# Kernel tuning notes

Measured on AMD Instinct MI355X. Metric: run time of the kernel, lower is better.

## Reference

```python
import jax, jax.numpy as jnp
import numpy as np

D_MODEL = 1024
NUM_HEADS = 16
HEAD_DIM = D_MODEL // NUM_HEADS


def setup_inputs() -> dict:
    key = jax.random.key(0)
    ks = jax.random.split(key, 9)
    s = 1.0 / np.sqrt(D_MODEL)
    x = jax.random.normal(ks[0], (2, 2048, D_MODEL), dtype=jnp.float32)
    Wq = jax.random.normal(ks[1], (D_MODEL, D_MODEL), dtype=jnp.float32) * s
    bq = jnp.zeros((D_MODEL,), dtype=jnp.float32)
    Wk = jax.random.normal(ks[2], (D_MODEL, D_MODEL), dtype=jnp.float32) * s
    bk = jnp.zeros((D_MODEL,), dtype=jnp.float32)
    Wv = jax.random.normal(ks[3], (D_MODEL, D_MODEL), dtype=jnp.float32) * s
    bv = jnp.zeros((D_MODEL,), dtype=jnp.float32)
    Wo = jax.random.normal(ks[4], (D_MODEL, D_MODEL), dtype=jnp.float32) * s
    bo = jnp.zeros((D_MODEL,), dtype=jnp.float32)
    return {"x": x, "Wq": Wq, "bq": bq, "Wk": Wk, "bk": bk,
            "Wv": Wv, "bv": bv, "Wo": Wo, "bo": bo}


def reference(x, Wq, bq, Wk, bk, Wv, bv, Wo, bo):
    B, S, D = x.shape
    H, Hd = NUM_HEADS, HEAD_DIM
    scale = 1.0 / np.sqrt(Hd)

    def split_heads(t):  # [B,S,D] -> [B,H,S,Hd]
        return t.reshape(B, S, H, Hd).transpose(0, 2, 1, 3)

    q = split_heads(x @ Wq + bq)
    k = split_heads(x @ Wk + bk)
    v = split_heads(x @ Wv + bv)

    scores = jnp.einsum('bhqd,bhkd->bhqk', q, k) * scale
    scores = scores - jnp.max(scores, axis=-1, keepdims=True)
    attn = jax.nn.softmax(scores, axis=-1)
    attended = jnp.einsum('bhqk,bhkd->bhqd', attn, v)
    attended = attended.transpose(0, 2, 1, 3).reshape(B, S, D)
    return attended @ Wo + bo
```

## Files before the change

### kernel.cpp

```cpp
#include <hip/hip_runtime.h>
#include <hip/hip_bf16.h>

typedef __bf16 bf16_t;
typedef __bf16 bf16x8 __attribute__((ext_vector_type(8)));
typedef __bf16 bf16x4 __attribute__((ext_vector_type(4)));
typedef float floatx4 __attribute__((ext_vector_type(4)));
typedef short short4v __attribute__((ext_vector_type(4)));

#define D_MODEL 1024
#define SEQ     2048
#define BATCH   2
#define NHEAD   16
#define HDIM    64
#define MTOT    (BATCH * SEQ)

#define QSCALE  0.18033688011112042f

union PBu { bf16x4 b; short4v s; };

__device__ __forceinline__ void async_copy16(const bf16_t* g, bf16_t* l) {
    __builtin_amdgcn_global_load_lds(
        (const __attribute__((address_space(1))) void*)g,
        (__attribute__((address_space(3))) void*)l, 16, 0, 0);
}

__global__ void prep_kernel(
    const float* __restrict__ x, bf16_t* __restrict__ xb,
    const float* __restrict__ W0, const float* __restrict__ W1,
    const float* __restrict__ W2, const float* __restrict__ W3,
    bf16_t* __restrict__ T0, bf16_t* __restrict__ T1,
    bf16_t* __restrict__ T2, bf16_t* __restrict__ T3)
{
    const int z = blockIdx.z;
    const int tx = threadIdx.x, ty = threadIdx.y;
    if (z == 4) {
        const int lin = (blockIdx.y * 32 + blockIdx.x) * 256 + ty * 32 + tx;
        const int base = lin * 16;
#pragma unroll
        for (int c = 0; c < 4; ++c) {
            const float4 v = *(const float4*)(x + base + c * 4);
            bf16x4 o = { (bf16_t)v.x, (bf16_t)v.y, (bf16_t)v.z, (bf16_t)v.w };
            *(bf16x4*)(xb + base + c * 4) = o;
        }
        return;
    }
    __shared__ float tile[32][33];
    const float* W = (z == 0) ? W0 : (z == 1) ? W1 : (z == 2) ? W2 : W3;
    bf16_t*     Wt = (z == 0) ? T0 : (z == 1) ? T1 : (z == 2) ? T2 : T3;
    const int k0 = blockIdx.y * 32, n0 = blockIdx.x * 32;
#pragma unroll
    for (int j = 0; j < 32; j += 8)
        tile[ty + j][tx] = W[(size_t)(k0 + ty + j) * D_MODEL + n0 + tx];
    __syncthreads();
#pragma unroll
    for (int j = 0; j < 32; j += 8)
        Wt[(size_t)(n0 + ty + j) * D_MODEL + k0 + tx] = (bf16_t)tile[tx][ty + j];
}

__device__ __forceinline__ void gemm_mainloop(
    const bf16_t* __restrict__ A, const bf16_t* __restrict__ Bt,
    int m0, int n0, bf16_t* As, bf16_t* Bs, floatx4 acc[4][4])
{
    const int tid  = threadIdx.x;
    const int lane = tid & 63;
    const int wid  = tid >> 6;
    const int quad = lane >> 4;
    const int col  = lane & 15;
    const int wm   = (wid >> 1) * 64;
    const int wn   = (wid & 1) * 64;
    const int srow = tid >> 3;
    const int scc  = ((tid & 7) ^ (srow & 7)) * 8;
    const int xorc = col & 7;

    const bf16_t* Ag = A  + (size_t)(m0 + srow) * D_MODEL + scc;
    const bf16_t* Bg = Bt + (size_t)(n0 + srow) * D_MODEL + scc;
    bf16_t* Al = As + tid * 8;
    bf16_t* Bl = Bs + tid * 8;

    for (int kb = 0; kb < D_MODEL; kb += 64) {
#pragma unroll
        for (int p = 0; p < 4; ++p) {
            async_copy16(Ag + kb + p * (32 * D_MODEL), Al + p * 2048);
            async_copy16(Bg + kb + p * (32 * D_MODEL), Bl + p * 2048);
        }
        __syncthreads();
#pragma unroll
        for (int kh = 0; kh < 2; ++kh) {
            bf16x8 af[4], bfr[4];
#pragma unroll
            for (int i = 0; i < 4; ++i)
                af[i] = *(const bf16x8*)(As + (wm + i * 16 + col) * 64 + (((kh * 4 + quad) ^ xorc) * 8));
#pragma unroll
            for (int j = 0; j < 4; ++j)
                bfr[j] = *(const bf16x8*)(Bs + (wn + j * 16 + col) * 64 + (((kh * 4 + quad) ^ xorc) * 8));
#pragma unroll
            for (int i = 0; i < 4; ++i)
#pragma unroll
                for (int j = 0; j < 4; ++j)
                    acc[i][j] = __builtin_amdgcn_mfma_f32_16x16x32_bf16(af[i], bfr[j], acc[i][j], 0, 0, 0);
        }
        __syncthreads();
    }
}

__global__ __launch_bounds__(256, 3) void gemm_qkv(
    const bf16_t* __restrict__ xb,
    const bf16_t* __restrict__ Wtq, const bf16_t* __restrict__ Wtk, const bf16_t* __restrict__ Wtv,
    const float* __restrict__ bq, const float* __restrict__ bk, const float* __restrict__ bv,
    bf16_t* __restrict__ Q, bf16_t* __restrict__ Kh, bf16_t* __restrict__ Vt)
{
    __shared__ bf16_t As[128 * 64];
    __shared__ bf16_t Bs[128 * 64];
    const int z = blockIdx.z;
    const bf16_t* Bt   = (z == 0) ? Wtq : (z == 1) ? Wtk : Wtv;
    const float*  bias = (z == 0) ? bq  : (z == 1) ? bk  : bv;
    bf16_t*       O    = (z == 0) ? Q   : (z == 1) ? Kh  : Vt;
    const float   qs   = (z == 0) ? QSCALE : 1.0f;
    const int m0 = blockIdx.y * 128;
    const int n0 = blockIdx.x * 128;

    floatx4 acc[4][4];
#pragma unroll
    for (int i = 0; i < 4; ++i)
#pragma unroll
        for (int j = 0; j < 4; ++j)
            acc[i][j] = (floatx4){0.f, 0.f, 0.f, 0.f};

    gemm_mainloop(xb, Bt, m0, n0, As, Bs, acc);

    const int tid  = threadIdx.x;
    const int lane = tid & 63;
    const int wid  = tid >> 6;
    const int quad = lane >> 4;
    const int col  = lane & 15;
    const int wm   = (wid >> 1) * 64;
    const int wn   = (wid & 1) * 64;

    if (z == 2) {
#pragma unroll
        for (int i = 0; i < 4; ++i) {
#pragma unroll
            for (int j = 0; j < 4; ++j) {
                const int n = n0 + wn + j * 16 + col;
                const float bb = bias[n];
                const int mb = m0 + wm + i * 16 + quad * 4;
                const size_t bhb = (size_t)((mb >> 11) * NHEAD + (n >> 6)) * (SEQ * HDIM);
                bf16x4 pk = { (bf16_t)(acc[i][j][0] + bb), (bf16_t)(acc[i][j][1] + bb),
                              (bf16_t)(acc[i][j][2] + bb), (bf16_t)(acc[i][j][3] + bb) };
                *(bf16x4*)(O + bhb + (size_t)(n & 63) * SEQ + (mb & 2047)) = pk;
            }
        }
    } else {
#pragma unroll
        for (int i = 0; i < 4; ++i) {
#pragma unroll
            for (int j = 0; j < 4; ++j) {
                const int n = n0 + wn + j * 16 + col;
                const float bb = bias[n];
#pragma unroll
                for (int r = 0; r < 4; ++r) {
                    const int m = m0 + wm + i * 16 + quad * 4 + r;
                    const float v = (acc[i][j][r] + bb) * qs;
                    const size_t bhb = (size_t)((m >> 11) * NHEAD + (n >> 6)) * (SEQ * HDIM);
                    O[bhb + (size_t)(m & 2047) * HDIM + (n & 63)] = (bf16_t)v;
                }
            }
        }
    }
}

__global__ __launch_bounds__(256, 4) void attn_kernel(
    const bf16_t* __restrict__ Q, const bf16_t* __restrict__ K,
    const bf16_t* __restrict__ Vt, bf16_t* __restrict__ A2)
{
    __shared__ bf16_t Ks[2][64 * 64];
    __shared__ bf16_t Vs[2][64 * 64];

    const int tid  = threadIdx.x;
    const int lane = tid & 63;
    const int wid  = tid >> 6;
    const int quad = lane >> 4;
    const int col  = lane & 15;
    const int xorc = col & 7;

    const int blk = blockIdx.x;
    const int idx = blk >> 3;
    const int bh  = (blk & 7) * 4 + (idx >> 5);
    const int q0  = (idx & 31) * 64;
    const int b   = bh >> 4, h = bh & 15;

    const bf16_t* Qb = Q  + (size_t)bh * (SEQ * HDIM);
    const bf16_t* Kb = K  + (size_t)bh * (SEQ * HDIM);
    const bf16_t* Vb = Vt + (size_t)bh * (SEQ * HDIM);

    const int qrow = q0 + wid * 16 + col;
    bf16x8 qf0 = *(const bf16x8*)(Qb + (size_t)qrow * HDIM + quad * 8);
    bf16x8 qf1 = *(const bf16x8*)(Qb + (size_t)qrow * HDIM + 32 + quad * 8);

    floatx4 o_acc[4];
    float lsum = 0.f;
#pragma unroll
    for (int dt = 0; dt < 4; ++dt)
        o_acc[dt] = (floatx4){0.f, 0.f, 0.f, 0.f};

    const int srow = tid >> 3;
    const int scc  = ((tid & 7) ^ (srow & 7)) * 8;
    const bf16_t* Kg = Kb + (size_t)srow * HDIM + scc;
    const bf16_t* Vg = Vb + (size_t)srow * SEQ + scc;

    async_copy16(Kg, &Ks[0][tid * 8]);
    async_copy16(Kg + (size_t)32 * HDIM, &Ks[0][2048 + tid * 8]);
    async_copy16(Vg, &Vs[0][tid * 8]);
    async_copy16(Vg + (size_t)32 * SEQ, &Vs[0][2048 + tid * 8]);
    __syncthreads();

    for (int it = 0; it < 32; ++it) {
        const int cur = it & 1, nxt = cur ^ 1;
        if (it + 1 < 32) {
            const int ko = (it + 1) * 64;
            async_copy16(Kg + (size_t)ko * HDIM, &Ks[nxt][tid * 8]);
            async_copy16(Kg + (size_t)(ko + 32) * HDIM, &Ks[nxt][2048 + tid * 8]);
            async_copy16(Vg + ko, &Vs[nxt][tid * 8]);
            async_copy16(Vg + (size_t)32 * SEQ + ko, &Vs[nxt][2048 + tid * 8]);
        }
        const bf16_t* Kc = Ks[cur];
        const bf16_t* Vc = Vs[cur];

        bf16x8 kf[4][2];
#pragma unroll
        for (int t = 0; t < 4; ++t) {
            kf[t][0] = *(const bf16x8*)(Kc + (t * 16 + col) * 64 + ((quad ^ xorc) * 8));
            kf[t][1] = *(const bf16x8*)(Kc + (t * 16 + col) * 64 + (((4 + quad) ^ xorc) * 8));
        }
        short4v vfr[4][4];
#pragma unroll
        for (int dt = 0; dt < 4; ++dt)
#pragma unroll
            for (int t = 0; t < 4; ++t) {
                const int sch = t * 2 + (quad >> 1);
                vfr[dt][t] = *(const short4v*)(Vc + (dt * 16 + col) * 64 + ((sch ^ xorc) * 8) + (quad & 1) * 4);
            }

        floatx4 s_acc[4];
        short4v pb[4];
#pragma unroll
        for (int t = 0; t < 4; ++t) {
            s_acc[t] = (floatx4){0.f, 0.f, 0.f, 0.f};
            s_acc[t] = __builtin_amdgcn_mfma_f32_16x16x32_bf16(kf[t][0], qf0, s_acc[t], 0, 0, 0);
            s_acc[t] = __builtin_amdgcn_mfma_f32_16x16x32_bf16(kf[t][1], qf1, s_acc[t], 0, 0, 0);
        }
#pragma unroll
        for (int t = 0; t < 4; ++t) {
            const float p0 = __builtin_amdgcn_exp2f(s_acc[t][0]);
            const float p1 = __builtin_amdgcn_exp2f(s_acc[t][1]);
            const float p2 = __builtin_amdgcn_exp2f(s_acc[t][2]);
            const float p3 = __builtin_amdgcn_exp2f(s_acc[t][3]);
            lsum += (p0 + p1) + (p2 + p3);
            PBu u;
            u.b = (bf16x4){ (bf16_t)p0, (bf16_t)p1, (bf16_t)p2, (bf16_t)p3 };
            pb[t] = u.s;
        }
#pragma unroll
        for (int dt = 0; dt < 4; ++dt)
#pragma unroll
            for (int t = 0; t < 4; ++t)
                o_acc[dt] = __builtin_amdgcn_mfma_f32_16x16x16bf16_1k(vfr[dt][t], pb[t], o_acc[dt], 0, 0, 0);
        __syncthreads();
    }

    lsum += __shfl_xor(lsum, 16, 64);
    lsum += __shfl_xor(lsum, 32, 64);
    const float inv = 1.0f / lsum;

    bf16_t* dst = A2 + ((size_t)(b * SEQ + qrow)) * D_MODEL + h * HDIM + quad * 4;
#pragma unroll
    for (int dt = 0; dt < 4; ++dt) {
        bf16x4 pk = { (bf16_t)(o_acc[dt][0] * inv), (bf16_t)(o_acc[dt][1] * inv),
                      (bf16_t)(o_acc[dt][2] * inv), (bf16_t)(o_acc[dt][3] * inv) };
        *(bf16x4*)(dst + dt * 16) = pk;
    }
}

__global__ __launch_bounds__(256, 3) void gemm_proj(
    const bf16_t* __restrict__ A2, const bf16_t* __restrict__ Wto,
    const float* __restrict__ bo, float* __restrict__ out)
{
    __shared__ bf16_t As[64 * 64];
    __shared__ bf16_t Bs[128 * 64];
    const int m0 = blockIdx.y * 64;
    const int n0 = blockIdx.x * 128;

    const int tid  = threadIdx.x;
    const int lane = tid & 63;
    const int wid  = tid >> 6;
    const int quad = lane >> 4;
    const int col  = lane & 15;
    const int wm   = (wid >> 1) * 32;
    const int wn   = (wid & 1) * 64;
    const int srow = tid >> 3;
    const int scc  = ((tid & 7) ^ (srow & 7)) * 8;
    const int xorc = col & 7;

    floatx4 acc[2][4];
#pragma unroll
    for (int i = 0; i < 2; ++i)
#pragma unroll
        for (int j = 0; j < 4; ++j)
            acc[i][j] = (floatx4){0.f, 0.f, 0.f, 0.f};

    const bf16_t* Ag = A2  + (size_t)(m0 + srow) * D_MODEL + scc;
    const bf16_t* Bg = Wto + (size_t)(n0 + srow) * D_MODEL + scc;
    bf16_t* Al = As + tid * 8;
    bf16_t* Bl = Bs + tid * 8;

    for (int kb = 0; kb < D_MODEL; kb += 64) {
#pragma unroll
        for (int p = 0; p < 2; ++p)
            async_copy16(Ag + kb + p * (32 * D_MODEL), Al + p * 2048);
#pragma unroll
        for (int p = 0; p < 4; ++p)
            async_copy16(Bg + kb + p * (32 * D_MODEL), Bl + p * 2048);
        __syncthreads();
#pragma unroll
        for (int kh = 0; kh < 2; ++kh) {
            bf16x8 af[2], bfr[4];
#pragma unroll
            for (int i = 0; i < 2; ++i)
                af[i] = *(const bf16x8*)(As + (wm + i * 16 + col) * 64 + (((kh * 4 + quad) ^ xorc) * 8));
#pragma unroll
            for (int j = 0; j < 4; ++j)
                bfr[j] = *(const bf16x8*)(Bs + (wn + j * 16 + col) * 64 + (((kh * 4 + quad) ^ xorc) * 8));
#pragma unroll
            for (int i = 0; i < 2; ++i)
#pragma unroll
                for (int j = 0; j < 4; ++j)
                    acc[i][j] = __builtin_amdgcn_mfma_f32_16x16x32_bf16(af[i], bfr[j], acc[i][j], 0, 0, 0);
        }
        __syncthreads();
    }

#pragma unroll
    for (int i = 0; i < 2; ++i) {
#pragma unroll
        for (int j = 0; j < 4; ++j) {
            const int n = n0 + wn + j * 16 + col;
            const float bb = bo[n];
#pragma unroll
            for (int r = 0; r < 4; ++r) {
                const int m = m0 + wm + i * 16 + quad * 4 + r;
                out[(size_t)m * D_MODEL + n] = acc[i][j][r] + bb;
            }
        }
    }
}

extern "C" void kernel_launch(void* const* d_in, const int* in_sizes, int n_in,
                              void* d_out, int out_size, void* d_ws, size_t ws_size,
                              hipStream_t stream) {
    const float* x  = (const float*)d_in[0];
    const float* Wq = (const float*)d_in[1];
    const float* bq = (const float*)d_in[2];
    const float* Wk = (const float*)d_in[3];
    const float* bk = (const float*)d_in[4];
    const float* Wv = (const float*)d_in[5];
    const float* bv = (const float*)d_in[6];
    const float* Wo = (const float*)d_in[7];
    const float* bo = (const float*)d_in[8];
    float* out = (float*)d_out;

    const size_t MB = 1ull << 20;
    char* ws = (char*)d_ws;
    bf16_t* Q     = (bf16_t*)(ws + 0 * MB);
    bf16_t* Kh    = (bf16_t*)(ws + 8 * MB);
    bf16_t* Vt    = (bf16_t*)(ws + 16 * MB);
    bf16_t* A2    = (bf16_t*)(ws + 24 * MB);
    bf16_t* xb    = (bf16_t*)(ws + 32 * MB);
    bf16_t* Wtq   = (bf16_t*)(ws + 40 * MB);
    bf16_t* Wtk   = (bf16_t*)(ws + 42 * MB);
    bf16_t* Wtv   = (bf16_t*)(ws + 44 * MB);
    bf16_t* Wto   = (bf16_t*)(ws + 46 * MB);

    prep_kernel<<<dim3(32, 32, 5), dim3(32, 8), 0, stream>>>(
        x, xb, Wq, Wk, Wv, Wo, Wtq, Wtk, Wtv, Wto);

    gemm_qkv<<<dim3(D_MODEL / 128, MTOT / 128, 3), 256, 0, stream>>>(
        xb, Wtq, Wtk, Wtv, bq, bk, bv, Q, Kh, Vt);

    attn_kernel<<<dim3(1024), 256, 0, stream>>>(Q, Kh, Vt, A2);

    gemm_proj<<<dim3(D_MODEL / 128, MTOT / 64), 256, 0, stream>>>(A2, Wto, bo, out);
}
```

Measured before the change: 193.2 us.

## Process two query sub-tiles per wave and drop K/V double buffering in attention

The attention kernel now runs with 128 threads (2 waves), each wave handling 32 query rows as two 16-row sub-tiles. Each K/V fragment read from shared memory is reused across twice as many queries. The double-buffered async K/V prefetch is replaced by a single buffer that is loaded and then synchronised at the start of each iteration. This halves LDS use and fragment loads per query, but it exposes global load latency with no overlap and adds register pressure.

```diff
diff --git a/kernel.cpp b/kernel.cpp
--- a/kernel.cpp
+++ b/kernel.cpp
@@ -169,12 +169,12 @@
     }
 }
 
-__global__ __launch_bounds__(256, 4) void attn_kernel(
+__global__ __launch_bounds__(128, 4) void attn_kernel(
     const bf16_t* __restrict__ Q, const bf16_t* __restrict__ K,
     const bf16_t* __restrict__ Vt, bf16_t* __restrict__ A2)
 {
-    __shared__ bf16_t Ks[2][64 * 64];
-    __shared__ bf16_t Vs[2][64 * 64];
+    __shared__ bf16_t Ks[64 * 64];
+    __shared__ bf16_t Vs[64 * 64];
 
     const int tid  = threadIdx.x;
     const int lane = tid & 63;
@@ -193,44 +193,43 @@
     const bf16_t* Kb = K  + (size_t)bh * (SEQ * HDIM);
     const bf16_t* Vb = Vt + (size_t)bh * (SEQ * HDIM);
 
-    const int qrow = q0 + wid * 16 + col;
-    bf16x8 qf0 = *(const bf16x8*)(Qb + (size_t)qrow * HDIM + quad * 8);
-    bf16x8 qf1 = *(const bf16x8*)(Qb + (size_t)qrow * HDIM + 32 + quad * 8);
-
-    floatx4 o_acc[4];
-    float lsum = 0.f;
-#pragma unroll
-    for (int dt = 0; dt < 4; ++dt)
-        o_acc[dt] = (floatx4){0.f, 0.f, 0.f, 0.f};
+    bf16x8 qf[2][2];
+#pragma unroll
+    for (int st = 0; st < 2; ++st) {
+        const int qrow = q0 + wid * 32 + st * 16 + col;
+        qf[st][0] = *(const bf16x8*)(Qb + (size_t)qrow * HDIM + quad * 8);
+        qf[st][1] = *(const bf16x8*)(Qb + (size_t)qrow * HDIM + 32 + quad * 8);
+    }
+
+    floatx4 o_acc[2][4];
+    float lsum[2] = {0.f, 0.f};
+#pragma unroll
+    for (int st = 0; st < 2; ++st)
+#pragma unroll
+        for (int dt = 0; dt < 4; ++dt)
+            o_acc[st][dt] = (floatx4){0.f, 0.f, 0.f, 0.f};
 
     const int srow = tid >> 3;
     const int scc  = ((tid & 7) ^ (srow & 7)) * 8;
     const bf16_t* Kg = Kb + (size_t)srow * HDIM + scc;
     const bf16_t* Vg = Vb + (size_t)srow * SEQ + scc;
-
-    async_copy16(Kg, &Ks[0][tid * 8]);
-    async_copy16(Kg + (size_t)32 * HDIM, &Ks[0][2048 + tid * 8]);
-    async_copy16(Vg, &Vs[0][tid * 8]);
-    async_copy16(Vg + (size_t)32 * SEQ, &Vs[0][2048 + tid * 8]);
-    __syncthreads();
+    bf16_t* KsL = Ks + tid * 8;
+    bf16_t* VsL = Vs + tid * 8;
 
     for (int it = 0; it < 32; ++it) {
-        const int cur = it & 1, nxt = cur ^ 1;
-        if (it + 1 < 32) {
-            const int ko = (it + 1) * 64;
-            async_copy16(Kg + (size_t)ko * HDIM, &Ks[nxt][tid * 8]);
-            async_copy16(Kg + (size_t)(ko + 32) * HDIM, &Ks[nxt][2048 + tid * 8]);
-            async_copy16(Vg + ko, &Vs[nxt][tid * 8]);
-            async_copy16(Vg + (size_t)32 * SEQ + ko, &Vs[nxt][2048 + tid * 8]);
-        }
-        const bf16_t* Kc = Ks[cur];
-        const bf16_t* Vc = Vs[cur];
+        const int ko = it * 64;
+#pragma unroll
+        for (int p = 0; p < 4; ++p) {
+            async_copy16(Kg + (size_t)(ko + p * 16) * HDIM, KsL + p * 1024);
+            async_copy16(Vg + (size_t)(p * 16) * SEQ + ko, VsL + p * 1024);
+        }
+        __syncthreads();
 
         bf16x8 kf[4][2];
 #pragma unroll
         for (int t = 0; t < 4; ++t) {
-            kf[t][0] = *(const bf16x8*)(Kc + (t * 16 + col) * 64 + ((quad ^ xorc) * 8));
-            kf[t][1] = *(const bf16x8*)(Kc + (t * 16 + col) * 64 + (((4 + quad) ^ xorc) * 8));
+            kf[t][0] = *(const bf16x8*)(Ks + (t * 16 + col) * 64 + ((quad ^ xorc) * 8));
+            kf[t][1] = *(const bf16x8*)(Ks + (t * 16 + col) * 64 + (((4 + quad) ^ xorc) * 8));
         }
         short4v vfr[4][4];
 #pragma unroll
@@ -238,46 +237,56 @@
 #pragma unroll
             for (int t = 0; t < 4; ++t) {
                 const int sch = t * 2 + (quad >> 1);
-                vfr[dt][t] = *(const short4v*)(Vc + (dt * 16 + col) * 64 + ((sch ^ xorc) * 8) + (quad & 1) * 4);
-            }
-
-        floatx4 s_acc[4];
-        short4v pb[4];
-#pragma unroll
-        for (int t = 0; t < 4; ++t) {
-            s_acc[t] = (floatx4){0.f, 0.f, 0.f, 0.f};
-            s_acc[t] = __builtin_amdgcn_mfma_f32_16x16x32_bf16(kf[t][0], qf0, s_acc[t], 0, 0, 0);
-            s_acc[t] = __builtin_amdgcn_mfma_f32_16x16x32_bf16(kf[t][1], qf1, s_acc[t], 0, 0, 0);
-        }
-#pragma unroll
-        for (int t = 0; t < 4; ++t) {
-            const float p0 = __builtin_amdgcn_exp2f(s_acc[t][0]);
-            const float p1 = __builtin_amdgcn_exp2f(s_acc[t][1]);
-            const float p2 = __builtin_amdgcn_exp2f(s_acc[t][2]);
-            const float p3 = __builtin_amdgcn_exp2f(s_acc[t][3]);
-            lsum += (p0 + p1) + (p2 + p3);
-            PBu u;
-            u.b = (bf16x4){ (bf16_t)p0, (bf16_t)p1, (bf16_t)p2, (bf16_t)p3 };
-            pb[t] = u.s;
-        }
-#pragma unroll
-        for (int dt = 0; dt < 4; ++dt)
-#pragma unroll
-            for (int t = 0; t < 4; ++t)
-                o_acc[dt] = __builtin_amdgcn_mfma_f32_16x16x16bf16_1k(vfr[dt][t], pb[t], o_acc[dt], 0, 0, 0);
-        __syncthreads();
-    }
-
-    lsum += __shfl_xor(lsum, 16, 64);
-    lsum += __shfl_xor(lsum, 32, 64);
-    const float inv = 1.0f / lsum;
-
-    bf16_t* dst = A2 + ((size_t)(b * SEQ + qrow)) * D_MODEL + h * HDIM + quad * 4;
-#pragma unroll
-    for (int dt = 0; dt < 4; ++dt) {
-        bf16x4 pk = { (bf16_t)(o_acc[dt][0] * inv), (bf16_t)(o_acc[dt][1] * inv),
-                      (bf16_t)(o_acc[dt][2] * inv), (bf16_t)(o_acc[dt][3] * inv) };
-        *(bf16x4*)(dst + dt * 16) = pk;
+                vfr[dt][t] = *(const short4v*)(Vs + (dt * 16 + col) * 64 + ((sch ^ xorc) * 8) + (quad & 1) * 4);
+            }
+
+#pragma unroll
+        for (int st = 0; st < 2; ++st) {
+            floatx4 s_acc[4];
+            short4v pb[4];
+#pragma unroll
+            for (int t = 0; t < 4; ++t) {
+                s_acc[t] = (floatx4){0.f, 0.f, 0.f, 0.f};
+                s_acc[t] = __builtin_amdgcn_mfma_f32_16x16x32_bf16(kf[t][0], qf[st][0], s_acc[t], 0, 0, 0);
+                s_acc[t] = __builtin_amdgcn_mfma_f32_16x16x32_bf16(kf[t][1], qf[st][1], s_acc[t], 0, 0, 0);
+            }
+#pragma unroll
+            for (int t = 0; t < 4; ++t) {
+                const float p0 = __builtin_amdgcn_exp2f(s_acc[t][0]);
+                const float p1 = __builtin_amdgcn_exp2f(s_acc[t][1]);
+                const float p2 = __builtin_amdgcn_exp2f(s_acc[t][2]);
+                const float p3 = __builtin_amdgcn_exp2f(s_acc[t][3]);
+                lsum[st] += (p0 + p1) + (p2 + p3);
+                PBu u;
+                u.b = (bf16x4){ (bf16_t)p0, (bf16_t)p1, (bf16_t)p2, (bf16_t)p3 };
+                pb[t] = u.s;
+            }
+#pragma unroll
+            for (int dt = 0; dt < 4; ++dt)
+#pragma unroll
+                for (int t = 0; t < 4; ++t)
+                    o_acc[st][dt] = __builtin_amdgcn_mfma_f32_16x16x16bf16_1k(vfr[dt][t], pb[t], o_acc[st][dt], 0, 0, 0);
+        }
+        __syncthreads();
+    }
+
+#pragma unroll
+    for (int st = 0; st < 2; ++st) {
+        lsum[st] += __shfl_xor(lsum[st], 16, 64);
+        lsum[st] += __shfl_xor(lsum[st], 32, 64);
+    }
+
+#pragma unroll
+    for (int st = 0; st < 2; ++st) {
+        const float inv = 1.0f / lsum[st];
+        const int qrow = q0 + wid * 32 + st * 16 + col;
+        bf16_t* dst = A2 + ((size_t)(b * SEQ + qrow)) * D_MODEL + h * HDIM + quad * 4;
+#pragma unroll
+        for (int dt = 0; dt < 4; ++dt) {
+            bf16x4 pk = { (bf16_t)(o_acc[st][dt][0] * inv), (bf16_t)(o_acc[st][dt][1] * inv),
+                          (bf16_t)(o_acc[st][dt][2] * inv), (bf16_t)(o_acc[st][dt][3] * inv) };
+            *(bf16x4*)(dst + dt * 16) = pk;
+        }
     }
 }
 
@@ -386,7 +395,7 @@
     gemm_qkv<<<dim3(D_MODEL / 128, MTOT / 128, 3), 256, 0, stream>>>(
         xb, Wtq, Wtk, Wtv, bq, bk, bv, Q, Kh, Vt);
 
-    attn_kernel<<<dim3(1024), 256, 0, stream>>>(Q, Kh, Vt, A2);
+    attn_kernel<<<dim3(1024), 128, 0, stream>>>(Q, Kh, Vt, A2);
 
     gemm_proj<<<dim3(D_MODEL / 128, MTOT / 64), 256, 0, stream>>>(A2, Wto, bo, out);
 }
```

Result: no change. 190.9 us (-1.2%).
